# Kernel optimization log

Hardware: AMD Instinct MI355X
Metric: run time of the kernel (lower is better)

Reference implementation:

```python
import jax, jax.numpy as jnp
import numpy as np

P = 5.0
A = 10.0
NUM_VARS = 1_000_000
NUM_CLAUSES = 1_000_000
E = 3_000_000  # edges per polarity


def setup_inputs() -> dict:
    key = jax.random.key(0)
    k1, k2, k3, k4, k5 = jax.random.split(key, 5)
    xv = jax.random.uniform(k1, (NUM_VARS, 1), dtype=jnp.float32)
    # clause rows: shuffled arange % NUM_CLAUSES so every clause is non-empty
    cp = jax.random.permutation(k2, jnp.arange(E, dtype=jnp.int64) % NUM_CLAUSES)
    cn = jax.random.permutation(k3, jnp.arange(E, dtype=jnp.int64) % NUM_CLAUSES)
    vp = jax.random.randint(k4, (E,), 0, NUM_VARS, dtype=jnp.int64)
    vn = jax.random.randint(k5, (E,), 0, NUM_VARS, dtype=jnp.int64)
    adj_pos = jnp.stack([cp, vp])  # [2, E]
    adj_neg = jnp.stack([cn, vn])  # [2, E]
    clause_count = jnp.ones((NUM_CLAUSES,), dtype=jnp.float32)
    return {"xv": xv, "adj_pos": adj_pos, "adj_neg": adj_neg, "clause_count": clause_count}


def reference(xv, adj_pos, adj_neg, clause_count):
    x = xv.reshape(-1)            # [V]
    xn = 1.0 - x
    # gather literal values and their exp(p*.) weights along edges
    lit = jnp.concatenate([x[adj_pos[1]], xn[adj_neg[1]]])            # [2E]
    xe = jnp.concatenate([jnp.exp(P * x)[adj_pos[1]], jnp.exp(P * xn)[adj_neg[1]]])  # [2E]
    idx = jnp.concatenate([adj_pos[0], adj_neg[0]])                   # [2E]
    numerator = jax.ops.segment_sum(lit * xe, idx, num_segments=NUM_CLAUSES)
    dominator = jax.ops.segment_sum(xe, idx, num_segments=NUM_CLAUSES)
    # push_to_side: 1/(1+exp(a*(0.5-x))) == sigmoid(a*(x-0.5))
    sm = jax.nn.sigmoid(A * (numerator / dominator - 0.5))            # [NUM_CLAUSES]
    # metric = mse_loss(sm, clause_count)
    loss = jnp.mean((sm - clause_count) ** 2)
    return loss
```

## Files before the change

### kernel.cpp

```cpp
#include <hip/hip_runtime.h>

constexpr int   NUM_CLAUSES = 1000000;
constexpr int   NUM_EDGES   = 3000000;
constexpr float Pc = 5.0f;
constexpr float Ac = 10.0f;

constexpr float FXSCALE = 64.0f;
constexpr float FXINV   = 1.0f / 64.0f;

constexpr int NB  = 250;
constexpr int CPB = 4000;
constexpr int CAP = CPB * 6;

constexpr int RPB   = 4096;
constexpr int RPT   = 16;
constexpr int NBLKP = (NUM_EDGES + RPB - 1) / RPB;

constexpr float QSCALE = 1048575.0f;
constexpr float QINV   = 1.0f / 1048575.0f;

constexpr size_t OFF_CTR = 24000000;
constexpr size_t OFF_PAR = 24001024;

__device__ __forceinline__ unsigned pack_fx(float num, float den) {
    unsigned lo = (unsigned)(num * FXSCALE + 0.5f);
    unsigned hi = (unsigned)(den * FXSCALE + 0.5f);
    return lo | (hi << 16);
}

__global__ __launch_bounds__(256)
void partition_kernel(const int*   __restrict__ adj_pos,
                      const int*   __restrict__ adj_neg,
                      const float* __restrict__ x,
                      unsigned* __restrict__ recs,
                      unsigned* __restrict__ counters) {
    __shared__ unsigned hist[NB];
    __shared__ unsigned base[NB];

    const bool neg   = (blockIdx.x >= (unsigned)NBLKP);
    const int  sblk  = neg ? (int)blockIdx.x - NBLKP : (int)blockIdx.x;
    const int  start = sblk * RPB;
    const int  n     = min(RPB, NUM_EDGES - start);
    const int* crow  = neg ? adj_neg : adj_pos;
    const int* vrow  = crow + NUM_EDGES;

    for (int b = threadIdx.x; b < NB; b += 256) hist[b] = 0;
    __syncthreads();

    unsigned rec[RPT];
    unsigned meta[RPT];

    #pragma unroll
    for (int j = 0; j < RPT / 4; ++j) {
        const int r0 = (j * 256 + (int)threadIdx.x) * 4;
        int4 c4, v4;
        const bool full = (r0 + 3 < n);
        if (full) {
            c4 = ((const int4*)(crow + start))[j * 256 + threadIdx.x];
            v4 = ((const int4*)(vrow + start))[j * 256 + threadIdx.x];
        }
        #pragma unroll
        for (int k = 0; k < 4; ++k) {
            const int rr = j * 4 + k;
            meta[rr] = 0xFFFFFFFFu;
            if (full || (r0 + k < n)) {
                const int i = start + r0 + k;
                int c = full ? (&c4.x)[k] : crow[i];
                int v = full ? (&v4.x)[k] : vrow[i];
                int b = c / CPB;
                float xv  = x[v];
                float lit = neg ? (1.0f - xv) : xv;
                unsigned q = (unsigned)(lit * QSCALE + 0.5f);
                rec[rr] = (q << 12) | (unsigned)(c - b * CPB);
                unsigned rank = atomicAdd(&hist[b], 1u);
                meta[rr] = ((unsigned)b << 12) | rank;
            }
        }
    }
    __syncthreads();

    for (int b = threadIdx.x; b < NB; b += 256) {
        unsigned h = hist[b];
        base[b] = h ? atomicAdd(&counters[b], h) : 0u;
    }
    __syncthreads();

    #pragma unroll
    for (int rr = 0; rr < RPT; ++rr) {
        unsigned m = meta[rr];
        if (m != 0xFFFFFFFFu) {
            unsigned b    = m >> 12;
            unsigned rank = m & 0xFFFu;
            recs[(size_t)b * CAP + base[b] + rank] = rec[rr];
        }
    }
}

__global__ __launch_bounds__(1024)
void bucket_loss_kernel(const uint4* __restrict__ recs4,
                        const float* __restrict__ cc,
                        float* __restrict__ partials) {
    __shared__ unsigned lacc[CPB];
    const int b = blockIdx.x;
    for (int j = threadIdx.x; j < CPB; j += 1024) lacc[j] = 0;
    __syncthreads();

    const uint4* r4 = recs4 + (size_t)b * (CAP / 4);
    for (int k = threadIdx.x; k < CAP / 4; k += 1024) {
        uint4 e = r4[k];
        #pragma unroll
        for (int k2 = 0; k2 < 4; ++k2) {
            unsigned r  = (&e.x)[k2];
            float lit = (float)(r >> 12) * QINV;
            float w   = __expf(Pc * lit);
            atomicAdd(&lacc[r & 0xFFFu], pack_fx(lit * w, w));
        }
    }
    __syncthreads();

    float v = 0.0f;
    const float* gc = cc + (size_t)b * CPB;
    for (int j = threadIdx.x; j < CPB; j += 1024) {
        unsigned a   = lacc[j];
        float    num = (float)(a & 0xffffu) * FXINV;
        float    den = (float)(a >> 16)     * FXINV;
        float    sm  = 1.0f / (1.0f + __expf(-Ac * (num / den - 0.5f)));
        float    e0  = sm - gc[j];
        v += e0 * e0;
    }
    v *= 1.0f / (float)NUM_CLAUSES;

    #pragma unroll
    for (int off = 32; off > 0; off >>= 1)
        v += __shfl_down(v, off, 64);

    __shared__ float partial[16];
    int lane = threadIdx.x & 63;
    int wid  = threadIdx.x >> 6;
    if (lane == 0) partial[wid] = v;
    __syncthreads();
    if (threadIdx.x == 0) {
        float s = 0.f;
        #pragma unroll
        for (int w = 0; w < 16; ++w) s += partial[w];
        partials[b] = s;
    }
}

__global__ void final_kernel(const float* __restrict__ partials,
                             float* __restrict__ out, int n) {
    float v = 0.0f;
    for (int i = threadIdx.x; i < n; i += 256) v += partials[i];

    #pragma unroll
    for (int off = 32; off > 0; off >>= 1)
        v += __shfl_down(v, off, 64);

    __shared__ float partial[4];
    int lane = threadIdx.x & 63;
    int wid  = threadIdx.x >> 6;
    if (lane == 0) partial[wid] = v;
    __syncthreads();
    if (threadIdx.x == 0)
        out[0] = partial[0] + partial[1] + partial[2] + partial[3];
}

extern "C" void kernel_launch(void* const* d_in, const int* in_sizes, int n_in,
                              void* d_out, int out_size, void* d_ws, size_t ws_size,
                              hipStream_t stream) {
    const float* xv      = (const float*)d_in[0];
    const int*   adj_pos = (const int*)  d_in[1];
    const int*   adj_neg = (const int*)  d_in[2];
    const float* cc      = (const float*)d_in[3];

    char* ws = (char*)d_ws;
    unsigned* recs     = (unsigned*)ws;
    unsigned* counters = (unsigned*)(ws + OFF_CTR);
    float*    partials = (float*)   (ws + OFF_PAR);
    float*    out      = (float*)d_out;

    hipMemsetAsync(counters, 0, NB * sizeof(unsigned), stream);

    partition_kernel<<<2 * NBLKP, 256, 0, stream>>>(adj_pos, adj_neg, xv,
                                                    recs, counters);

    bucket_loss_kernel<<<NB, 1024, 0, stream>>>((const uint4*)recs, cc, partials);

    final_kernel<<<1, 256, 0, stream>>>(partials, out, NB);
}
```

Baseline: 167.7 us.

## Stage partitioned records in shared memory for bucket-contiguous global writes

The partition kernel now builds a block-local prefix scan over bucket histograms, places the records into shared memory sorted by bucket, and then writes them out with consecutive threads covering consecutive positions. Before, each thread scattered its records straight to global memory. The goal is to make writes within a bucket run contiguously and coalesce, and to issue all x gathers before the atomics for more memory-level parallelism. Blocks grow to 512 threads and 8192 records, which costs about 41KB of LDS per block and may lower occupancy.

```diff
diff --git a/kernel.cpp b/kernel.cpp
--- a/kernel.cpp
+++ b/kernel.cpp
@@ -12,8 +12,9 @@
 constexpr int CPB = 4000;
 constexpr int CAP = CPB * 6;
 
-constexpr int RPB   = 4096;
-constexpr int RPT   = 16;
+constexpr int TPB   = 512;
+constexpr int RPB   = 8192;
+constexpr int RPT   = RPB / TPB;
 constexpr int NBLKP = (NUM_EDGES + RPB - 1) / RPB;
 
 constexpr float QSCALE = 1048575.0f;
@@ -28,14 +29,19 @@
     return lo | (hi << 16);
 }
 
-__global__ __launch_bounds__(256)
+__global__ __launch_bounds__(TPB)
 void partition_kernel(const int*   __restrict__ adj_pos,
                       const int*   __restrict__ adj_neg,
                       const float* __restrict__ x,
                       unsigned* __restrict__ recs,
                       unsigned* __restrict__ counters) {
-    __shared__ unsigned hist[NB];
-    __shared__ unsigned base[NB];
+    __shared__ unsigned      hist[NB];
+    __shared__ unsigned      sbase[NB];
+    __shared__ unsigned      lbase[NB];
+    __shared__ unsigned      srec[RPB];
+    __shared__ unsigned char sbid[RPB];
+    __shared__ unsigned      wsum[TPB / 64];
+    __shared__ unsigned      woff[TPB / 64];
 
     const bool neg   = (blockIdx.x >= (unsigned)NBLKP);
     const int  sblk  = neg ? (int)blockIdx.x - NBLKP : (int)blockIdx.x;
@@ -43,56 +49,85 @@
     const int  n     = min(RPB, NUM_EDGES - start);
     const int* crow  = neg ? adj_neg : adj_pos;
     const int* vrow  = crow + NUM_EDGES;
-
-    for (int b = threadIdx.x; b < NB; b += 256) hist[b] = 0;
-    __syncthreads();
-
-    unsigned rec[RPT];
-    unsigned meta[RPT];
-
-    #pragma unroll
-    for (int j = 0; j < RPT / 4; ++j) {
-        const int r0 = (j * 256 + (int)threadIdx.x) * 4;
-        int4 c4, v4;
-        const bool full = (r0 + 3 < n);
-        if (full) {
-            c4 = ((const int4*)(crow + start))[j * 256 + threadIdx.x];
-            v4 = ((const int4*)(vrow + start))[j * 256 + threadIdx.x];
-        }
-        #pragma unroll
-        for (int k = 0; k < 4; ++k) {
-            const int rr = j * 4 + k;
-            meta[rr] = 0xFFFFFFFFu;
-            if (full || (r0 + k < n)) {
-                const int i = start + r0 + k;
-                int c = full ? (&c4.x)[k] : crow[i];
-                int v = full ? (&v4.x)[k] : vrow[i];
-                int b = c / CPB;
-                float xv  = x[v];
-                float lit = neg ? (1.0f - xv) : xv;
-                unsigned q = (unsigned)(lit * QSCALE + 0.5f);
-                rec[rr] = (q << 12) | (unsigned)(c - b * CPB);
-                unsigned rank = atomicAdd(&hist[b], 1u);
-                meta[rr] = ((unsigned)b << 12) | rank;
-            }
-        }
-    }
-    __syncthreads();
-
-    for (int b = threadIdx.x; b < NB; b += 256) {
-        unsigned h = hist[b];
-        base[b] = h ? atomicAdd(&counters[b], h) : 0u;
-    }
-    __syncthreads();
-
-    #pragma unroll
-    for (int rr = 0; rr < RPT; ++rr) {
-        unsigned m = meta[rr];
-        if (m != 0xFFFFFFFFu) {
-            unsigned b    = m >> 12;
-            unsigned rank = m & 0xFFFu;
-            recs[(size_t)b * CAP + base[b] + rank] = rec[rr];
-        }
+    const int  tid   = (int)threadIdx.x;
+
+    for (int b = tid; b < NB; b += TPB) hist[b] = 0;
+    __syncthreads();
+
+    int cc_[RPT], vv_[RPT];
+    if (n == RPB) {
+        #pragma unroll
+        for (int j = 0; j < RPT / 4; ++j) {
+            int4 c4 = ((const int4*)(crow + start))[j * TPB + tid];
+            int4 v4 = ((const int4*)(vrow + start))[j * TPB + tid];
+            cc_[4*j] = c4.x; cc_[4*j+1] = c4.y; cc_[4*j+2] = c4.z; cc_[4*j+3] = c4.w;
+            vv_[4*j] = v4.x; vv_[4*j+1] = v4.y; vv_[4*j+2] = v4.z; vv_[4*j+3] = v4.w;
+        }
+    } else {
+        #pragma unroll
+        for (int r = 0; r < RPT; ++r) {
+            int pos = 4 * ((r >> 2) * TPB + tid) + (r & 3);
+            cc_[r] = (pos < n) ? crow[start + pos] : -1;
+            vv_[r] = (pos < n) ? vrow[start + pos] : 0;
+        }
+    }
+
+    float xv[RPT];
+    #pragma unroll
+    for (int r = 0; r < RPT; ++r) xv[r] = x[vv_[r]];
+
+    unsigned rec[RPT], meta[RPT];
+    #pragma unroll
+    for (int r = 0; r < RPT; ++r) {
+        meta[r] = 0xFFFFFFFFu;
+        if (cc_[r] >= 0) {
+            int   c   = cc_[r];
+            int   b   = c / CPB;
+            float lit = neg ? (1.0f - xv[r]) : xv[r];
+            unsigned q = (unsigned)(lit * QSCALE + 0.5f);
+            rec[r] = (q << 12) | (unsigned)(c - b * CPB);
+            unsigned rank = atomicAdd(&hist[b], 1u);
+            meta[r] = ((unsigned)b << 13) | rank;
+        }
+    }
+    __syncthreads();
+
+    unsigned h    = (tid < NB) ? hist[tid] : 0u;
+    unsigned incl = h;
+    #pragma unroll
+    for (int off = 1; off < 64; off <<= 1) {
+        unsigned t = __shfl_up(incl, off, 64);
+        if ((tid & 63) >= off) incl += t;
+    }
+    if ((tid & 63) == 63) wsum[tid >> 6] = incl;
+    __syncthreads();
+    if (tid == 0) {
+        unsigned a = 0;
+        #pragma unroll
+        for (int w = 0; w < TPB / 64; ++w) { woff[w] = a; a += wsum[w]; }
+    }
+    __syncthreads();
+    if (tid < NB) {
+        lbase[tid] = incl - h + woff[tid >> 6];
+        sbase[tid] = h ? atomicAdd(&counters[tid], h) : 0u;
+    }
+    __syncthreads();
+
+    #pragma unroll
+    for (int r = 0; r < RPT; ++r) {
+        if (meta[r] != 0xFFFFFFFFu) {
+            unsigned b    = meta[r] >> 13;
+            unsigned rank = meta[r] & 0x1FFFu;
+            unsigned p    = lbase[b] + rank;
+            srec[p] = rec[r];
+            sbid[p] = (unsigned char)b;
+        }
+    }
+    __syncthreads();
+
+    for (int p = tid; p < n; p += TPB) {
+        unsigned b = sbid[p];
+        recs[(size_t)b * CAP + sbase[b] + ((unsigned)p - lbase[b])] = srec[p];
     }
 }
 
@@ -181,7 +216,7 @@
 
     hipMemsetAsync(counters, 0, NB * sizeof(unsigned), stream);
 
-    partition_kernel<<<2 * NBLKP, 256, 0, stream>>>(adj_pos, adj_neg, xv,
+    partition_kernel<<<2 * NBLKP, TPB, 0, stream>>>(adj_pos, adj_neg, xv,
                                                     recs, counters);
 
     bucket_loss_kernel<<<NB, 1024, 0, stream>>>((const uint4*)recs, cc, partials);
```

Result: faster. 145.2 us (-13.4%).
